# Performance work log

Measured on AMD Instinct MI355X. Metric: run time of the kernel, lower is better.

The kernel has to match this reference:

```python
import jax, jax.numpy as jnp
import numpy as np

N_NODES = 100000
N_EDGES = 1600000
D_IN = 128
D_OUT = 128


def setup_inputs() -> dict:
    key = jax.random.key(0)
    k1, k2, k3, k4, k5, k6 = jax.random.split(key, 6)
    x = jax.random.normal(k1, (N_NODES, D_IN), dtype=jnp.float32)
    edge_index = jax.random.randint(k2, (2, N_EDGES), 0, N_NODES, dtype=jnp.int64)
    edge_weight = jax.random.uniform(k3, (N_EDGES,), dtype=jnp.float32)
    # Linear(in_features=128, out_features=128, bias=True) parameters
    bound = 1.0 / np.sqrt(D_IN)
    W = jax.random.uniform(k4, (D_OUT, D_IN), minval=-bound, maxval=bound, dtype=jnp.float32)
    b = jax.random.uniform(k5, (D_OUT,), minval=-bound, maxval=bound, dtype=jnp.float32)
    return {
        "x": x,
        "edge_index": edge_index,
        "edge_weight": edge_weight,
        "W": W,
        "b": b,
        "vertex_cnt": N_NODES,
        "rule_cnt": 0,
    }


def reference(x, edge_index, edge_weight, W, b, vertex_cnt, rule_cnt):
    # KPropagate: edge-based message passing.
    # messages[e] = edge_weight[e] * x[src[e]]; out[dst] = sum of messages into dst.
    src = edge_index[0]
    dst = edge_index[1]
    msgs = x[src] * edge_weight[:, None]          # [E, D_IN]
    agg = jax.ops.segment_sum(msgs, dst, num_segments=vertex_cnt)  # [N, D_IN]
    # Dense linear projection: y = agg @ W^T + b
    return agg @ W.T + b
```

## Files before the change

kernel.cpp:

```cpp
#include <hip/hip_runtime.h>
#include <hip/hip_bf16.h>

#define D 128
#define RT 64
#define BK 64
#define CAP 2048
#define SUBCAP 256
#define PAD 16

typedef __attribute__((ext_vector_type(8))) short short8;
typedef __attribute__((ext_vector_type(4))) float floatx4;

__device__ __forceinline__ ushort f2bf(float v) {
  return __hip_bfloat16_raw(__float2bfloat16(v)).x;
}
__device__ __forceinline__ float bf2f(ushort u) {
  return __uint_as_float((unsigned)u << 16);
}

__device__ __forceinline__ int xcd_id() {
  int v;
  asm volatile("s_getreg_b32 %0, hwreg(HW_REG_XCC_ID)" : "=s"(v));
  return v & 7;
}

__global__ __launch_bounds__(256) void prep_w(const float* __restrict__ W,
                                              ushort* __restrict__ Wp) {
  int g = blockIdx.x * 256 + threadIdx.x;
  int ct = g >> 8;
  int ks = (g >> 6) & 3;
  int lane = g & 63;
  int m = lane & 15;
  int q = lane >> 4;
  const float* p = W + (ct * 16 + m) * 128 + ks * 32 + q * 8;
  float4 v0 = *(const float4*)p;
  float4 v1 = *(const float4*)(p + 4);
  *(ushort4*)(Wp + (long long)g * 8) =
      make_ushort4(f2bf(v0.x), f2bf(v0.y), f2bf(v0.z), f2bf(v0.w));
  *(ushort4*)(Wp + (long long)g * 8 + 4) =
      make_ushort4(f2bf(v1.x), f2bf(v1.y), f2bf(v1.z), f2bf(v1.w));
}

__global__ __launch_bounds__(256) void k1_gemm_fill(
    const float* __restrict__ x, const ushort* __restrict__ Wp,
    ushort* __restrict__ y, const int* __restrict__ ei,
    const float* __restrict__ ew, int* __restrict__ cursor,
    int2* __restrict__ bucket, int N, int E, int GB) {
  if (blockIdx.x >= GB) {
    int sb = xcd_id();
    int e = (blockIdx.x - GB) * 256 + threadIdx.x;
    if (e < E) {
      int s = __builtin_nontemporal_load(ei + e);
      int d = __builtin_nontemporal_load(ei + E + e);
      float w = __builtin_nontemporal_load(ew + e);
      int bk = d >> 6;
      int p = atomicAdd(&cursor[(bk * 8 + sb) * PAD], 1);
      if (p < SUBCAP)
        bucket[(long long)bk * CAP + sb * SUBCAP + p] =
            make_int2(s | ((d & 63) << 26), __float_as_int(w));
    }
    return;
  }
  __shared__ __align__(16) ushort sX[RT * 136];

  int tid = threadIdx.x;
  int rowBase = blockIdx.x * RT;

#pragma unroll
  for (int it = 0; it < 8; it++) {
    int i = tid + it * 256;
    int r = i >> 5;
    int c4 = i & 31;
    int row = rowBase + r;
    floatx4 v;
    if (row < N)
      v = __builtin_nontemporal_load(
          (const floatx4*)(x + (long long)row * 128 + c4 * 4));
    else
      v = (floatx4){0.f, 0.f, 0.f, 0.f};
    *(ushort4*)&sX[r * 136 + c4 * 4] =
        make_ushort4(f2bf(v.x), f2bf(v.y), f2bf(v.z), f2bf(v.w));
  }
  __syncthreads();

  int wv = tid >> 6;
  int lane = tid & 63;
  int m = lane & 15;
  int q = lane >> 4;

  const ushort* aRow = &sX[(wv * 16 + m) * 136 + q * 8];
  const ushort* wBase = Wp + (long long)lane * 8;

  floatx4 acc[8];
#pragma unroll
  for (int ct = 0; ct < 8; ct++) acc[ct] = (floatx4){0.f, 0.f, 0.f, 0.f};

#pragma unroll
  for (int ks = 0; ks < 4; ks++) {
    short8 a = *(const short8*)(aRow + ks * 32);
#pragma unroll
    for (int ct = 0; ct < 8; ct++) {
      short8 b = *(const short8*)(wBase + (ct * 256 + ks * 64) * 8);
      acc[ct] = __builtin_amdgcn_mfma_f32_16x16x32_bf16(a, b, acc[ct], 0, 0, 0);
    }
  }

  int row0 = rowBase + wv * 16 + q * 4;
#pragma unroll
  for (int r = 0; r < 4; r++) {
    int row = row0 + r;
    if (row < N) {
      ushort* yp = y + (long long)row * 128 + m;
#pragma unroll
      for (int ct = 0; ct < 8; ct++) yp[ct * 16] = f2bf(acc[ct][r]);
    }
  }
}

__global__ __launch_bounds__(256) void sort_gather(
    const ushort* __restrict__ y, const int2* __restrict__ bucket,
    const int* __restrict__ cursor, const float* __restrict__ bias,
    float* __restrict__ out, int N) {
  __shared__ __align__(16) int2 smd[CAP];
  __shared__ int sdeg[BK];
  __shared__ int soffs[BK];
  __shared__ int scur[BK];

  int tid = threadIdx.x;
  int bk = blockIdx.x;
  long long base = (long long)bk * CAP;

  if (tid < BK) sdeg[tid] = 0;
  __syncthreads();
#pragma unroll
  for (int sb = 0; sb < 8; sb++) {
    int c = min(cursor[(bk * 8 + sb) * PAD], SUBCAP);
    for (int i = tid; i < c; i += 256) {
      unsigned v = (unsigned)bucket[base + sb * SUBCAP + i].x;
      atomicAdd(&sdeg[v >> 26], 1);
    }
  }
  __syncthreads();
  if (tid < BK) {
    int s = 0;
    for (int j = 0; j < tid; j++) s += sdeg[j];
    soffs[tid] = s;
    scur[tid] = s;
  }
  __syncthreads();
#pragma unroll
  for (int sb = 0; sb < 8; sb++) {
    int c = min(cursor[(bk * 8 + sb) * PAD], SUBCAP);
    for (int i = tid; i < c; i += 256) {
      int2 md = bucket[base + sb * SUBCAP + i];
      int d = (unsigned)md.x >> 26;
      int pos = atomicAdd(&scur[d], 1);
      smd[pos] = md;
    }
  }
  __syncthreads();

  int wv = tid >> 6;
  int lane = tid & 63;
  const ushort2* yv = (const ushort2*)y;
  float2 bb = ((const float2*)bias)[lane];

  for (int nd = wv; nd < BK; nd += 4) {
    int node = bk * BK + nd;
    if (node >= N) continue;
    int st = soffs[nd];
    int c = sdeg[nd];
    float ax = 0.f, ay = 0.f;
    int j = 0;
    for (; j + 4 <= c; j += 4) {
      int2 m0 = smd[st + j];
      int2 m1 = smd[st + j + 1];
      int2 m2 = smd[st + j + 2];
      int2 m3 = smd[st + j + 3];
      int s0 = m0.x & 0x03FFFFFF, s1 = m1.x & 0x03FFFFFF;
      int s2 = m2.x & 0x03FFFFFF, s3 = m3.x & 0x03FFFFFF;
      float w0 = __int_as_float(m0.y), w1 = __int_as_float(m1.y);
      float w2 = __int_as_float(m2.y), w3 = __int_as_float(m3.y);
      ushort2 u0 = yv[(long long)s0 * 64 + lane];
      ushort2 u1 = yv[(long long)s1 * 64 + lane];
      ushort2 u2 = yv[(long long)s2 * 64 + lane];
      ushort2 u3 = yv[(long long)s3 * 64 + lane];
      ax += w0 * bf2f(u0.x) + w1 * bf2f(u1.x) + w2 * bf2f(u2.x) +
            w3 * bf2f(u3.x);
      ay += w0 * bf2f(u0.y) + w1 * bf2f(u1.y) + w2 * bf2f(u2.y) +
            w3 * bf2f(u3.y);
    }
    for (; j < c; j++) {
      int2 m0 = smd[st + j];
      int s0 = m0.x & 0x03FFFFFF;
      float w0 = __int_as_float(m0.y);
      ushort2 u0 = yv[(long long)s0 * 64 + lane];
      ax += w0 * bf2f(u0.x);
      ay += w0 * bf2f(u0.y);
    }
    float2 o = {ax + bb.x, ay + bb.y};
    ((float2*)out)[(long long)node * 64 + lane] = o;
  }
}

extern "C" void kernel_launch(void* const* d_in, const int* in_sizes, int n_in,
                              void* d_out, int out_size, void* d_ws,
                              size_t ws_size, hipStream_t stream) {
  const float* x = (const float*)d_in[0];
  const int* ei = (const int*)d_in[1];
  const float* ew = (const float*)d_in[2];
  const float* W = (const float*)d_in[3];
  const float* b = (const float*)d_in[4];

  int N = in_sizes[0] / D;
  int E = in_sizes[2];
  int NBK = (N + BK - 1) / BK;

  int* cursor = (int*)d_ws;
  ushort* Wp = (ushort*)(cursor + (size_t)NBK * 8 * PAD);
  int2* bucket = (int2*)(Wp + 128 * 128);
  ushort* y = (ushort*)(bucket + (size_t)NBK * CAP);

  (void)hipMemsetAsync(cursor, 0, (size_t)NBK * 8 * PAD * sizeof(int), stream);
  prep_w<<<8, 256, 0, stream>>>(W, Wp);

  int GB = (N + RT - 1) / RT;
  int FB = (E + 255) / 256;
  k1_gemm_fill<<<GB + FB, 256, 0, stream>>>(x, Wp, y, ei, ew, cursor, bucket,
                                            N, E, GB);
  sort_gather<<<NBK, 256, 0, stream>>>(y, bucket, cursor, b, (float*)d_out, N);
}
```

Before: 251.3 us.

## Fuse memset into weight prep and batch edges per thread in fill

Replaces the hipMemsetAsync with a zeroing branch inside the weight-packing kernel, which removes one launch. The edge-bucketing blocks now handle 8 edges per thread, issuing all loads first, then all atomics, then all stores, so more memory operations are in flight and far fewer fill blocks are needed. Fill blocks are moved ahead of the GEMM blocks in the grid so they are scheduled first. The trade-offs are more registers per fill thread and a different interleaving of atomic traffic with the GEMM work.

```diff
diff --git a/kernel.cpp b/kernel.cpp
--- a/kernel.cpp
+++ b/kernel.cpp
@@ -7,6 +7,7 @@
 #define CAP 2048
 #define SUBCAP 256
 #define PAD 16
+#define EPT 8
 
 typedef __attribute__((ext_vector_type(8))) short short8;
 typedef __attribute__((ext_vector_type(4))) float floatx4;
@@ -24,47 +25,72 @@
   return v & 7;
 }
 
-__global__ __launch_bounds__(256) void prep_w(const float* __restrict__ W,
-                                              ushort* __restrict__ Wp) {
-  int g = blockIdx.x * 256 + threadIdx.x;
-  int ct = g >> 8;
-  int ks = (g >> 6) & 3;
-  int lane = g & 63;
-  int m = lane & 15;
-  int q = lane >> 4;
-  const float* p = W + (ct * 16 + m) * 128 + ks * 32 + q * 8;
-  float4 v0 = *(const float4*)p;
-  float4 v1 = *(const float4*)(p + 4);
-  *(ushort4*)(Wp + (long long)g * 8) =
-      make_ushort4(f2bf(v0.x), f2bf(v0.y), f2bf(v0.z), f2bf(v0.w));
-  *(ushort4*)(Wp + (long long)g * 8 + 4) =
-      make_ushort4(f2bf(v1.x), f2bf(v1.y), f2bf(v1.z), f2bf(v1.w));
+__global__ __launch_bounds__(256) void init_ws(const float* __restrict__ W,
+                                               ushort* __restrict__ Wp,
+                                               int* __restrict__ cursor,
+                                               int NZ) {
+  int tid = threadIdx.x;
+  if (blockIdx.x < 8) {
+    int g = blockIdx.x * 256 + tid;
+    int ct = g >> 8;
+    int ks = (g >> 6) & 3;
+    int lane = g & 63;
+    int m = lane & 15;
+    int q = lane >> 4;
+    const float* p = W + (ct * 16 + m) * 128 + ks * 32 + q * 8;
+    float4 v0 = *(const float4*)p;
+    float4 v1 = *(const float4*)(p + 4);
+    *(ushort4*)(Wp + (long long)g * 8) =
+        make_ushort4(f2bf(v0.x), f2bf(v0.y), f2bf(v0.z), f2bf(v0.w));
+    *(ushort4*)(Wp + (long long)g * 8 + 4) =
+        make_ushort4(f2bf(v1.x), f2bf(v1.y), f2bf(v1.z), f2bf(v1.w));
+    return;
+  }
+  int idx = (blockIdx.x - 8) * 256 + tid;
+  if (idx < NZ) cursor[idx] = 0;
 }
 
 __global__ __launch_bounds__(256) void k1_gemm_fill(
     const float* __restrict__ x, const ushort* __restrict__ Wp,
     ushort* __restrict__ y, const int* __restrict__ ei,
     const float* __restrict__ ew, int* __restrict__ cursor,
-    int2* __restrict__ bucket, int N, int E, int GB) {
-  if (blockIdx.x >= GB) {
+    int2* __restrict__ bucket, int N, int E, int FB) {
+  int tid = threadIdx.x;
+  if (blockIdx.x < FB) {
     int sb = xcd_id();
-    int e = (blockIdx.x - GB) * 256 + threadIdx.x;
-    if (e < E) {
-      int s = __builtin_nontemporal_load(ei + e);
-      int d = __builtin_nontemporal_load(ei + E + e);
-      float w = __builtin_nontemporal_load(ew + e);
-      int bk = d >> 6;
-      int p = atomicAdd(&cursor[(bk * 8 + sb) * PAD], 1);
-      if (p < SUBCAP)
-        bucket[(long long)bk * CAP + sb * SUBCAP + p] =
-            make_int2(s | ((d & 63) << 26), __float_as_int(w));
+    long long e0 = (long long)blockIdx.x * (256 * EPT) + tid;
+    int md[EPT];
+    int bk[EPT];
+    float w[EPT];
+#pragma unroll
+    for (int k = 0; k < EPT; k++) {
+      long long e = e0 + k * 256;
+      if (e < E) {
+        int s = __builtin_nontemporal_load(ei + e);
+        int d = __builtin_nontemporal_load(ei + E + e);
+        w[k] = __builtin_nontemporal_load(ew + e);
+        bk[k] = d >> 6;
+        md[k] = s | ((d & 63) << 26);
+      }
+    }
+    int p[EPT];
+#pragma unroll
+    for (int k = 0; k < EPT; k++) {
+      long long e = e0 + k * 256;
+      if (e < E) p[k] = atomicAdd(&cursor[(bk[k] * 8 + sb) * PAD], 1);
+    }
+#pragma unroll
+    for (int k = 0; k < EPT; k++) {
+      long long e = e0 + k * 256;
+      if (e < E && p[k] < SUBCAP)
+        bucket[(long long)bk[k] * CAP + sb * SUBCAP + p[k]] =
+            make_int2(md[k], __float_as_int(w[k]));
     }
     return;
   }
   __shared__ __align__(16) ushort sX[RT * 136];
 
-  int tid = threadIdx.x;
-  int rowBase = blockIdx.x * RT;
+  int rowBase = (blockIdx.x - FB) * RT;
 
 #pragma unroll
   for (int it = 0; it < 8; it++) {
@@ -221,12 +247,13 @@
   int2* bucket = (int2*)(Wp + 128 * 128);
   ushort* y = (ushort*)(bucket + (size_t)NBK * CAP);
 
-  (void)hipMemsetAsync(cursor, 0, (size_t)NBK * 8 * PAD * sizeof(int), stream);
-  prep_w<<<8, 256, 0, stream>>>(W, Wp);
+  int NZ = NBK * 8 * PAD;
+  int ZB = (NZ + 255) / 256;
+  init_ws<<<8 + ZB, 256, 0, stream>>>(W, Wp, cursor, NZ);
 
   int GB = (N + RT - 1) / RT;
-  int FB = (E + 255) / 256;
-  k1_gemm_fill<<<GB + FB, 256, 0, stream>>>(x, Wp, y, ei, ew, cursor, bucket,
-                                            N, E, GB);
+  int FB = (E + 256 * EPT - 1) / (256 * EPT);
+  k1_gemm_fill<<<FB + GB, 256, 0, stream>>>(x, Wp, y, ei, ew, cursor, bucket,
+                                            N, E, FB);
   sort_gather<<<NBK, 256, 0, stream>>>(y, bucket, cursor, b, (float*)d_out, N);
 }
```

New measurement: 265.9 us. 5.8% more time.
